# Kernel optimization log

Hardware: AMD Instinct MI355X
Metric: run time of the kernel (lower is better)

The kernel has to match this reference:

```python
import jax, jax.numpy as jnp
import numpy as np

EMB = 512
HEADS = 8

def setup_inputs() -> dict:
    key = jax.random.key(0)
    ks = jax.random.split(key, 6)
    x = jax.random.normal(ks[0], (8, 1024, EMB), dtype=jnp.float32)
    s = EMB ** -0.5
    Wq = jax.random.normal(ks[1], (EMB, EMB), dtype=jnp.float32) * s
    Wk = jax.random.normal(ks[2], (EMB, EMB), dtype=jnp.float32) * s
    Wv = jax.random.normal(ks[3], (EMB, EMB), dtype=jnp.float32) * s
    ln_gamma = jnp.ones((EMB,), dtype=jnp.float32)
    ln_beta = jnp.zeros((EMB,), dtype=jnp.float32)
    return {"x": x, "Wq": Wq, "Wk": Wk, "Wv": Wv, "ln_gamma": ln_gamma, "ln_beta": ln_beta}

def reference(x, Wq, Wk, Wv, ln_gamma, ln_beta):
    B, S, E = x.shape
    H = HEADS
    D = E // H
    scale = E ** -0.5  # note: source scales by emb_size**-0.5, not head_dim
    # projections (bias=False, torch Linear: x @ W.T)
    q = (x @ Wq.T).reshape(B, S, H, D).transpose(0, 2, 1, 3)  # [B,H,S,D]
    k = (x @ Wk.T).reshape(B, S, H, D).transpose(0, 2, 1, 3)
    v = (x @ Wv.T).reshape(B, S, H, D).transpose(0, 2, 1, 3)
    attn = jnp.einsum('bhqd,bhkd->bhqk', q, k) * scale
    attn = jax.nn.softmax(attn, axis=-1)
    out = jnp.einsum('bhqk,bhkd->bhqd', attn, v)
    out = out.transpose(0, 2, 1, 3).reshape(B, S, E)
    # LayerNorm (eps=1e-5, torch default)
    mu = jnp.mean(out, axis=-1, keepdims=True)
    var = jnp.var(out, axis=-1, keepdims=True)
    out = (out - mu) * jax.lax.rsqrt(var + 1e-5) * ln_gamma + ln_beta
    return out
```

## Files before the change

kernel.cpp:

```cpp
#include <hip/hip_runtime.h>
#include <hip/hip_bf16.h>

typedef __bf16 bf16_t;
typedef __bf16 bf16x4 __attribute__((ext_vector_type(4)));
typedef __bf16 bf16x8 __attribute__((ext_vector_type(8)));
typedef float  f32x4  __attribute__((ext_vector_type(4)));
typedef short  short4v __attribute__((ext_vector_type(4)));

#define GLL(gp, lp) __builtin_amdgcn_global_load_lds((const __attribute__((address_space(1))) void*)(gp), (__attribute__((address_space(3))) void*)(lp), 16, 0, 0)

__device__ __forceinline__ f32x4 mfma16x16x16_bf16(bf16x4 a, bf16x4 b, f32x4 c) {
#if __has_builtin(__builtin_amdgcn_mfma_f32_16x16x16_bf16)
    return __builtin_amdgcn_mfma_f32_16x16x16_bf16(a, b, c, 0, 0, 0);
#else
    return __builtin_amdgcn_mfma_f32_16x16x16bf16_1k(__builtin_bit_cast(short4v, a), __builtin_bit_cast(short4v, b), c, 0, 0, 0);
#endif
}

__device__ __forceinline__ float fexp2(float x) {
#if __has_builtin(__builtin_amdgcn_exp2f)
    return __builtin_amdgcn_exp2f(x);
#else
    return exp2f(x);
#endif
}

__global__ __launch_bounds__(256) void cvt_kernel(const float* __restrict__ x,
                                                  const float* __restrict__ wq,
                                                  const float* __restrict__ wk,
                                                  const float* __restrict__ wv,
                                                  bf16_t* __restrict__ xb,
                                                  bf16_t* __restrict__ wall) {
    const int TOT4 = 1245184;
    for (int i = blockIdx.x * blockDim.x + threadIdx.x; i < TOT4; i += gridDim.x * blockDim.x) {
        const float* src; bf16_t* dst; int off;
        if (i < 1048576) { src = x; dst = xb; off = i; }
        else {
            int j = i - 1048576;
            int wsel = j >> 16;
            off = j & 65535;
            src = (wsel == 0) ? wq : ((wsel == 1) ? wk : wv);
            dst = wall + ((size_t)wsel << 18);
        }
        float4 v = *(const float4*)(src + (size_t)off * 4);
        bf16x4 o = { (bf16_t)v.x, (bf16_t)v.y, (bf16_t)v.z, (bf16_t)v.w };
        *(bf16x4*)(dst + (size_t)off * 4) = o;
    }
}

__global__ __launch_bounds__(256) void proj_kernel(const bf16_t* __restrict__ xb,
                                                   const bf16_t* __restrict__ wall,
                                                   bf16_t* __restrict__ Qb,
                                                   bf16_t* __restrict__ Kb,
                                                   bf16_t* __restrict__ Vt) {
    __shared__ char psm[34816];

    const int tid = threadIdx.x;
    const int w = tid >> 6, lane = tid & 63;
    const int bx = blockIdx.x;
    const int nb = bx % 12, mb = bx / 12;
    const int n0 = nb * 128, m0 = mb * 128;
    const int wn = w & 1, wm = w >> 1;
    const int l15 = lane & 15, g = lane >> 4;

    const int srow = w * 32 + (lane >> 2);
    const int kcol = (lane & 3) * 8;
    const bf16_t* wsrc0 = wall + (size_t)(n0 + srow) * 512 + kcol;
    const bf16_t* xsrc0 = xb + (size_t)(m0 + srow) * 512 + kcol;

    f32x4 acc[4][4] = {};

    {
        bf16_t* lw = (bf16_t*)(psm) + w * 1024;
        bf16_t* lx = (bf16_t*)(psm + 8192) + w * 1024;
        GLL(wsrc0, lw);
        GLL(wsrc0 + 8192, lw + 512);
        GLL(xsrc0, lx);
        GLL(xsrc0 + 8192, lx + 512);
    }
    __syncthreads();

    for (int kt = 0; kt < 16; ++kt) {
        const int buf = kt & 1;
        if (kt < 15) {
            const int ko = (kt + 1) * 32;
            bf16_t* lw = (bf16_t*)(psm + (buf ^ 1) * 16384) + w * 1024;
            bf16_t* lx = (bf16_t*)(psm + (buf ^ 1) * 16384 + 8192) + w * 1024;
            GLL(wsrc0 + ko, lw);
            GLL(wsrc0 + 8192 + ko, lw + 512);
            GLL(xsrc0 + ko, lx);
            GLL(xsrc0 + 8192 + ko, lx + 512);
        }
        const bf16_t* sW = (const bf16_t*)(psm + buf * 16384);
        const bf16_t* sX = (const bf16_t*)(psm + buf * 16384 + 8192);

        bf16x8 af[4], bfv[4];
#pragma unroll
        for (int ni = 0; ni < 4; ++ni)
            af[ni] = *(const bf16x8*)(sW + (wn * 64 + ni * 16 + l15) * 32 + g * 8);
#pragma unroll
        for (int mi = 0; mi < 4; ++mi)
            bfv[mi] = *(const bf16x8*)(sX + (wm * 64 + mi * 16 + l15) * 32 + g * 8);
#pragma unroll
        for (int ni = 0; ni < 4; ++ni)
#pragma unroll
            for (int mi = 0; mi < 4; ++mi)
                acc[ni][mi] = __builtin_amdgcn_mfma_f32_16x16x32_bf16(af[ni], bfv[mi], acc[ni][mi], 0, 0, 0);
        __syncthreads();
    }

    const int which = n0 >> 9;
    if (which < 2) {
        bf16_t* dst = (which == 0) ? Qb : Kb;
#pragma unroll
        for (int ni = 0; ni < 4; ++ni) {
#pragma unroll
            for (int mi = 0; mi < 4; ++mi) {
                int j = (n0 & 511) + wn * 64 + ni * 16 + g * 4;
                int h = j >> 6, dd = j & 63;
                int sb = m0 + wm * 64 + mi * 16 + l15;
                int b = sb >> 10, s = sb & 1023;
                bf16x4 o = { (bf16_t)acc[ni][mi][0], (bf16_t)acc[ni][mi][1],
                             (bf16_t)acc[ni][mi][2], (bf16_t)acc[ni][mi][3] };
                *(bf16x4*)(dst + ((size_t)((b * 8 + h) * 1024 + s)) * 64 + dd) = o;
            }
        }
    } else {
        bf16_t* ctile = (bf16_t*)psm;
#pragma unroll
        for (int ni = 0; ni < 4; ++ni)
#pragma unroll
            for (int mi = 0; mi < 4; ++mi)
#pragma unroll
                for (int r = 0; r < 4; ++r)
                    ctile[(wn * 64 + ni * 16 + g * 4 + r) * 136 + wm * 64 + mi * 16 + l15] =
                        (bf16_t)acc[ni][mi][r];
        __syncthreads();
        const int rr = tid >> 1, half = tid & 1;
        const int jv = (n0 & 511) + rr;
        const int hh = jv >> 6, dd = jv & 63;
        const int b = m0 >> 10, sb = (m0 & 1023) + half * 64;
        bf16_t* dst = Vt + ((size_t)((b * 8 + hh) * 64 + dd)) * 1024 + sb;
        const bf16_t* src = ctile + rr * 136 + half * 64;
#pragma unroll
        for (int u = 0; u < 8; ++u)
            *(bf16x8*)(dst + u * 8) = *(const bf16x8*)(src + u * 8);
    }
}

__global__ __launch_bounds__(512, 4) void attn_kernel(const bf16_t* __restrict__ Qb,
                                                      const bf16_t* __restrict__ Kb,
                                                      const bf16_t* __restrict__ Vt,
                                                      bf16_t* __restrict__ Ob) {
    __shared__ char smem[65536];
    const int tid = threadIdx.x;
    const int w = tid >> 6, lane = tid & 63;
    const int pipe = w >> 2, ws = w & 3;
    const int l15 = lane & 15, g = lane >> 4, l7 = lane & 7;

    const int bx = blockIdx.x;
    const int xcd = bx & 7, i = bx >> 3;
    const int head = xcd * 8 + (i & 7);
    const int qblk = i >> 3;
    const int q0 = qblk * 128 + ws * 32;

    const size_t hoff = (size_t)head << 16;
    const bf16_t* Qh = Qb + hoff;
    const char* Kh = (const char*)(Kb + hoff) + pipe * 65536;
    const char* Vh = (const char*)(Vt + hoff) + pipe * 1024;

    const float c2 = 0.06376390597f;

    bf16x8 qf[2][2];
#pragma unroll
    for (int qh = 0; qh < 2; ++qh) {
        const bf16_t* qp = Qh + (q0 + qh * 16 + l15) * 64 + g * 8;
        bf16x8 a = *(const bf16x8*)(qp);
        bf16x8 b = *(const bf16x8*)(qp + 32);
#pragma unroll
        for (int j = 0; j < 8; ++j) {
            a[j] = (bf16_t)((float)a[j] * c2);
            b[j] = (bf16_t)((float)b[j] * c2);
        }
        qf[qh][0] = a; qf[qh][1] = b;
    }

    const int srow = ws * 8 + (lane >> 3);
    const int sw16 = (l7 ^ ((lane >> 3) & 7)) << 4;
    const char* Ksrc = Kh + srow * 128 + sw16;
    const char* Vsrc = Vh + srow * 2048 + sw16;
    char* region = smem + pipe * 32768;
    char* dstK = region + ws * 1024;
    char* dstV = region + 8192 + ws * 1024;

    const int e0 = (l7 ^ g) << 4;
    const int f0 = (g << 3) ^ (l7 << 4);

    f32x4 oacc[2][4] = {};
    f32x4 dacc[2] = {};
    const bf16x4 ones = { (bf16_t)1.0f, (bf16_t)1.0f, (bf16_t)1.0f, (bf16_t)1.0f };
    const f32x4 minit = { -4.0f, -4.0f, -4.0f, -4.0f };

    GLL(Ksrc, dstK);
    GLL(Ksrc + 4096, dstK + 4096);
    GLL(Vsrc, dstV);
    GLL(Vsrc + 65536, dstV + 4096);
    __syncthreads();

    for (int c = 0; c < 8; ++c) {
        const int buf = c & 1;
        if (c < 7) {
            const int nbo = (buf ^ 1) * 16384;
            GLL(Ksrc + (c + 1) * 8192, dstK + nbo);
            GLL(Ksrc + (c + 1) * 8192 + 4096, dstK + nbo + 4096);
            GLL(Vsrc + (c + 1) * 128, dstV + nbo);
            GLL(Vsrc + (c + 1) * 128 + 65536, dstV + nbo + 4096);
        }
        const char* bK = region + buf * 16384;
        const char* bV = bK + 8192;

        bf16x4 pb[2][4];
#pragma unroll
        for (int sub = 0; sub < 4; ++sub) {
            const char* rowp = bK + (sub * 16 + l15) * 128;
            bf16x8 ka0 = *(const bf16x8*)(rowp + e0);
            bf16x8 ka1 = *(const bf16x8*)(rowp + (e0 ^ 64));
#pragma unroll
            for (int qh = 0; qh < 2; ++qh) {
                f32x4 st = __builtin_amdgcn_mfma_f32_16x16x32_bf16(ka0, qf[qh][0], minit, 0, 0, 0);
                st = __builtin_amdgcn_mfma_f32_16x16x32_bf16(ka1, qf[qh][1], st, 0, 0, 0);
                float p0 = fexp2(st[0]), p1 = fexp2(st[1]), p2 = fexp2(st[2]), p3 = fexp2(st[3]);
                bf16x4 pv = { (bf16_t)p0, (bf16_t)p1, (bf16_t)p2, (bf16_t)p3 };
                pb[qh][sub] = pv;
                dacc[qh] = mfma16x16x16_bf16(ones, pv, dacc[qh]);
            }
        }

#pragma unroll
        for (int dt = 0; dt < 4; ++dt) {
            const char* vrowp = bV + (dt * 16 + l15) * 128;
#pragma unroll
            for (int ks = 0; ks < 4; ++ks) {
                bf16x4 va = *(const bf16x4*)(vrowp + (f0 ^ (ks << 5)));
                oacc[0][dt] = mfma16x16x16_bf16(va, pb[0][ks], oacc[0][dt]);
                oacc[1][dt] = mfma16x16x16_bf16(va, pb[1][ks], oacc[1][dt]);
            }
        }
        __syncthreads();
    }

    if (pipe == 1) {
#pragma unroll
        for (int qh = 0; qh < 2; ++qh) {
#pragma unroll
            for (int dt = 0; dt < 4; ++dt)
                *(f32x4*)(smem + (((ws * 2 + qh) * 4) + dt) * 1024 + lane * 16) = oacc[qh][dt];
            *(f32x4*)(smem + 32768 + (ws * 2 + qh) * 1024 + lane * 16) = dacc[qh];
        }
    }
    __syncthreads();
    if (pipe == 0) {
        const int b = head >> 3, h = head & 7;
#pragma unroll
        for (int qh = 0; qh < 2; ++qh) {
            f32x4 dp = *(const f32x4*)(smem + 32768 + (ws * 2 + qh) * 1024 + lane * 16);
            const float inv = 1.0f / (dacc[qh][0] + dp[0]);
            const int s = q0 + qh * 16 + l15;
            bf16_t* op = Ob + ((size_t)(b * 1024 + s)) * 512 + h * 64 + g * 4;
#pragma unroll
            for (int dt = 0; dt < 4; ++dt) {
                f32x4 o2 = *(const f32x4*)(smem + (((ws * 2 + qh) * 4) + dt) * 1024 + lane * 16);
                f32x4 t = oacc[qh][dt] + o2;
                bf16x4 o = { (bf16_t)(t[0] * inv), (bf16_t)(t[1] * inv),
                             (bf16_t)(t[2] * inv), (bf16_t)(t[3] * inv) };
                *(bf16x4*)(op + dt * 16) = o;
            }
        }
    }
}

__global__ __launch_bounds__(256) void ln_kernel(const bf16_t* __restrict__ O,
                                                 const float* __restrict__ gamma,
                                                 const float* __restrict__ beta,
                                                 float* __restrict__ out) {
    const int w = threadIdx.x >> 6, lane = threadIdx.x & 63;
    const int row = blockIdx.x * 4 + w;
    const bf16_t* rp = O + (size_t)row * 512 + lane * 8;
    bf16x8 v8 = *(const bf16x8*)rp;
    float v[8];
    float sum = 0.0f, sq = 0.0f;
#pragma unroll
    for (int i = 0; i < 8; ++i) { v[i] = (float)v8[i]; sum += v[i]; sq += v[i] * v[i]; }
#pragma unroll
    for (int msk = 1; msk < 64; msk <<= 1) {
        sum += __shfl_xor(sum, msk);
        sq  += __shfl_xor(sq, msk);
    }
    const float mean = sum * (1.0f / 512.0f);
    const float var = sq * (1.0f / 512.0f) - mean * mean;
    const float rs = rsqrtf(var + 1e-5f);
    float4 g0 = *(const float4*)(gamma + lane * 8);
    float4 g1 = *(const float4*)(gamma + lane * 8 + 4);
    float4 b0 = *(const float4*)(beta + lane * 8);
    float4 b1 = *(const float4*)(beta + lane * 8 + 4);
    float* op = out + (size_t)row * 512 + lane * 8;
    float4 o0, o1;
    o0.x = (v[0] - mean) * rs * g0.x + b0.x;
    o0.y = (v[1] - mean) * rs * g0.y + b0.y;
    o0.z = (v[2] - mean) * rs * g0.z + b0.z;
    o0.w = (v[3] - mean) * rs * g0.w + b0.w;
    o1.x = (v[4] - mean) * rs * g1.x + b1.x;
    o1.y = (v[5] - mean) * rs * g1.y + b1.y;
    o1.z = (v[6] - mean) * rs * g1.z + b1.z;
    o1.w = (v[7] - mean) * rs * g1.w + b1.w;
    *(float4*)op = o0;
    *(float4*)(op + 4) = o1;
}

extern "C" void kernel_launch(void* const* d_in, const int* in_sizes, int n_in,
                              void* d_out, int out_size, void* d_ws, size_t ws_size,
                              hipStream_t stream) {
    const float* x  = (const float*)d_in[0];
    const float* wq = (const float*)d_in[1];
    const float* wk = (const float*)d_in[2];
    const float* wv = (const float*)d_in[3];
    const float* gamma = (const float*)d_in[4];
    const float* beta  = (const float*)d_in[5];
    float* out = (float*)d_out;

    char* ws = (char*)d_ws;
    bf16_t* xb   = (bf16_t*)(ws);
    bf16_t* wall = (bf16_t*)(ws + 8388608);
    bf16_t* Qb   = (bf16_t*)(ws + 9961472);
    bf16_t* Kb   = (bf16_t*)(ws + 18350080);
    bf16_t* Vt   = (bf16_t*)(ws + 26738688);
    bf16_t* Ob   = (bf16_t*)(ws + 35127296);

    hipLaunchKernelGGL(cvt_kernel,  dim3(1024), dim3(256), 0, stream, x, wq, wk, wv, xb, wall);
    hipLaunchKernelGGL(proj_kernel, dim3(768),  dim3(256), 0, stream, xb, wall, Qb, Kb, Vt);
    hipLaunchKernelGGL(attn_kernel, dim3(512),  dim3(512), 0, stream, Qb, Kb, Vt, Ob);
    hipLaunchKernelGGL(ln_kernel,   dim3(2048), dim3(256), 0, stream, Ob, gamma, beta, out);
}
```

Measured before the change: 67.08 us.

## Double attention query tile per block to reuse K/V loads across more rows

Each attention block now handles 256 query rows (64 per wave) instead of 128, halving the grid to 256 blocks so each K/V tile loaded into LDS serves twice as many queries. The P·V product is interleaved per key sub-tile instead of buffering all probabilities, and the cross-pipe reduction runs in two rounds to fit shared memory. This cuts K/V global traffic and LDS fills per query, at the cost of more registers (launch bounds lowered to 2 blocks) and fewer blocks for the 256 CUs.

Measured after the change: 65.77 us. About the same (-2.0%).

```diff
diff --git a/kernel.cpp b/kernel.cpp
--- a/kernel.cpp
+++ b/kernel.cpp
@@ -148,7 +148,7 @@
     }
 }
 
-__global__ __launch_bounds__(512, 4) void attn_kernel(const bf16_t* __restrict__ Qb,
+__global__ __launch_bounds__(512, 2) void attn_kernel(const bf16_t* __restrict__ Qb,
                                                       const bf16_t* __restrict__ Kb,
                                                       const bf16_t* __restrict__ Vt,
                                                       bf16_t* __restrict__ Ob) {
@@ -159,10 +159,9 @@
     const int l15 = lane & 15, g = lane >> 4, l7 = lane & 7;
 
     const int bx = blockIdx.x;
-    const int xcd = bx & 7, i = bx >> 3;
-    const int head = xcd * 8 + (i & 7);
-    const int qblk = i >> 3;
-    const int q0 = qblk * 128 + ws * 32;
+    const int head = (bx & 7) * 8 + ((bx >> 3) & 7);
+    const int qq = bx >> 6;
+    const int q0 = qq * 256 + ws * 64;
 
     const size_t hoff = (size_t)head << 16;
     const bf16_t* Qh = Qb + hoff;
@@ -171,18 +170,18 @@
 
     const float c2 = 0.06376390597f;
 
-    bf16x8 qf[2][2];
-#pragma unroll
-    for (int qh = 0; qh < 2; ++qh) {
+    bf16x8 qf[4][2];
+#pragma unroll
+    for (int qh = 0; qh < 4; ++qh) {
         const bf16_t* qp = Qh + (q0 + qh * 16 + l15) * 64 + g * 8;
         bf16x8 a = *(const bf16x8*)(qp);
-        bf16x8 b = *(const bf16x8*)(qp + 32);
+        bf16x8 bq = *(const bf16x8*)(qp + 32);
 #pragma unroll
         for (int j = 0; j < 8; ++j) {
             a[j] = (bf16_t)((float)a[j] * c2);
-            b[j] = (bf16_t)((float)b[j] * c2);
-        }
-        qf[qh][0] = a; qf[qh][1] = b;
+            bq[j] = (bf16_t)((float)bq[j] * c2);
+        }
+        qf[qh][0] = a; qf[qh][1] = bq;
     }
 
     const int srow = ws * 8 + (lane >> 3);
@@ -196,8 +195,8 @@
     const int e0 = (l7 ^ g) << 4;
     const int f0 = (g << 3) ^ (l7 << 4);
 
-    f32x4 oacc[2][4] = {};
-    f32x4 dacc[2] = {};
+    f32x4 oacc[4][4] = {};
+    f32x4 dacc[4] = {};
     const bf16x4 ones = { (bf16_t)1.0f, (bf16_t)1.0f, (bf16_t)1.0f, (bf16_t)1.0f };
     const f32x4 minit = { -4.0f, -4.0f, -4.0f, -4.0f };
 
@@ -219,63 +218,65 @@
         const char* bK = region + buf * 16384;
         const char* bV = bK + 8192;
 
-        bf16x4 pb[2][4];
 #pragma unroll
         for (int sub = 0; sub < 4; ++sub) {
             const char* rowp = bK + (sub * 16 + l15) * 128;
             bf16x8 ka0 = *(const bf16x8*)(rowp + e0);
             bf16x8 ka1 = *(const bf16x8*)(rowp + (e0 ^ 64));
-#pragma unroll
-            for (int qh = 0; qh < 2; ++qh) {
+            bf16x4 pb[4];
+#pragma unroll
+            for (int qh = 0; qh < 4; ++qh) {
                 f32x4 st = __builtin_amdgcn_mfma_f32_16x16x32_bf16(ka0, qf[qh][0], minit, 0, 0, 0);
                 st = __builtin_amdgcn_mfma_f32_16x16x32_bf16(ka1, qf[qh][1], st, 0, 0, 0);
-                float p0 = fexp2(st[0]), p1 = fexp2(st[1]), p2 = fexp2(st[2]), p3 = fexp2(st[3]);
-                bf16x4 pv = { (bf16_t)p0, (bf16_t)p1, (bf16_t)p2, (bf16_t)p3 };
-                pb[qh][sub] = pv;
+                bf16x4 pv = { (bf16_t)fexp2(st[0]), (bf16_t)fexp2(st[1]),
+                              (bf16_t)fexp2(st[2]), (bf16_t)fexp2(st[3]) };
+                pb[qh] = pv;
                 dacc[qh] = mfma16x16x16_bf16(ones, pv, dacc[qh]);
             }
-        }
-
-#pragma unroll
-        for (int dt = 0; dt < 4; ++dt) {
-            const char* vrowp = bV + (dt * 16 + l15) * 128;
-#pragma unroll
-            for (int ks = 0; ks < 4; ++ks) {
-                bf16x4 va = *(const bf16x4*)(vrowp + (f0 ^ (ks << 5)));
-                oacc[0][dt] = mfma16x16x16_bf16(va, pb[0][ks], oacc[0][dt]);
-                oacc[1][dt] = mfma16x16x16_bf16(va, pb[1][ks], oacc[1][dt]);
-            }
-        }
-        __syncthreads();
-    }
-
-    if (pipe == 1) {
-#pragma unroll
-        for (int qh = 0; qh < 2; ++qh) {
-#pragma unroll
-            for (int dt = 0; dt < 4; ++dt)
-                *(f32x4*)(smem + (((ws * 2 + qh) * 4) + dt) * 1024 + lane * 16) = oacc[qh][dt];
-            *(f32x4*)(smem + 32768 + (ws * 2 + qh) * 1024 + lane * 16) = dacc[qh];
-        }
-    }
-    __syncthreads();
-    if (pipe == 0) {
-        const int b = head >> 3, h = head & 7;
-#pragma unroll
-        for (int qh = 0; qh < 2; ++qh) {
-            f32x4 dp = *(const f32x4*)(smem + 32768 + (ws * 2 + qh) * 1024 + lane * 16);
-            const float inv = 1.0f / (dacc[qh][0] + dp[0]);
-            const int s = q0 + qh * 16 + l15;
-            bf16_t* op = Ob + ((size_t)(b * 1024 + s)) * 512 + h * 64 + g * 4;
 #pragma unroll
             for (int dt = 0; dt < 4; ++dt) {
-                f32x4 o2 = *(const f32x4*)(smem + (((ws * 2 + qh) * 4) + dt) * 1024 + lane * 16);
-                f32x4 t = oacc[qh][dt] + o2;
-                bf16x4 o = { (bf16_t)(t[0] * inv), (bf16_t)(t[1] * inv),
-                             (bf16_t)(t[2] * inv), (bf16_t)(t[3] * inv) };
-                *(bf16x4*)(op + dt * 16) = o;
-            }
-        }
+                bf16x4 va = *(const bf16x4*)(bV + (dt * 16 + l15) * 128 + (f0 ^ (sub << 5)));
+                oacc[0][dt] = mfma16x16x16_bf16(va, pb[0], oacc[0][dt]);
+                oacc[1][dt] = mfma16x16x16_bf16(va, pb[1], oacc[1][dt]);
+                oacc[2][dt] = mfma16x16x16_bf16(va, pb[2], oacc[2][dt]);
+                oacc[3][dt] = mfma16x16x16_bf16(va, pb[3], oacc[3][dt]);
+            }
+        }
+        __syncthreads();
+    }
+
+    const int b = head >> 3, h = head & 7;
+#pragma unroll
+    for (int r = 0; r < 2; ++r) {
+        if (pipe == 1) {
+#pragma unroll
+            for (int j = 0; j < 2; ++j) {
+                const int qh = r * 2 + j;
+#pragma unroll
+                for (int dt = 0; dt < 4; ++dt)
+                    *(f32x4*)(smem + ws * 8192 + j * 4096 + dt * 1024 + lane * 16) = oacc[qh][dt];
+                *(float*)(smem + 32768 + (ws * 2 + j) * 256 + lane * 4) = dacc[qh][0];
+            }
+        }
+        __syncthreads();
+        if (pipe == 0) {
+#pragma unroll
+            for (int j = 0; j < 2; ++j) {
+                const int qh = r * 2 + j;
+                const float dn = dacc[qh][0] + *(const float*)(smem + 32768 + (ws * 2 + j) * 256 + lane * 4);
+                const float inv = 1.0f / dn;
+                const int s = q0 + qh * 16 + l15;
+                bf16_t* op = Ob + ((size_t)(b * 1024 + s)) * 512 + h * 64 + g * 4;
+#pragma unroll
+                for (int dt = 0; dt < 4; ++dt) {
+                    f32x4 t = oacc[qh][dt] + *(const f32x4*)(smem + ws * 8192 + j * 4096 + dt * 1024 + lane * 16);
+                    bf16x4 o = { (bf16_t)(t[0] * inv), (bf16_t)(t[1] * inv),
+                                 (bf16_t)(t[2] * inv), (bf16_t)(t[3] * inv) };
+                    *(bf16x4*)(op + dt * 16) = o;
+                }
+            }
+        }
+        __syncthreads();
     }
 }
 
@@ -338,6 +339,6 @@
 
     hipLaunchKernelGGL(cvt_kernel,  dim3(1024), dim3(256), 0, stream, x, wq, wk, wv, xb, wall);
     hipLaunchKernelGGL(proj_kernel, dim3(768),  dim3(256), 0, stream, xb, wall, Qb, Kb, Vt);
-    hipLaunchKernelGGL(attn_kernel, dim3(512),  dim3(512), 0, stream, Qb, Kb, Vt, Ob);
+    hipLaunchKernelGGL(attn_kernel, dim3(256),  dim3(512), 0, stream, Qb, Kb, Vt, Ob);
     hipLaunchKernelGGL(ln_kernel,   dim3(2048), dim3(256), 0, stream, Ob, gamma, beta, out);
 }
```
